# Kernel tuning notes

Measured on AMD Instinct MI355X. Metric: run time of the kernel, lower is better.

Reference implementation:

```python
import jax, jax.numpy as jnp
import numpy as np

N_NODES = 100000
D_IN = 128
D_OUT = 128
N_EDGES = 1600000
BN_EPS = 1e-5
LEAKY_SLOPE = 0.01


def setup_inputs() -> dict:
    key = jax.random.key(0)
    ks = jax.random.split(key, 8)
    x = jax.random.normal(ks[0], (N_NODES, D_IN), dtype=jnp.float32)
    edge_index = jax.random.randint(ks[1], (2, N_EDGES), 0, N_NODES, dtype=jnp.int32)
    scale = 1.0 / np.sqrt(D_IN)
    W = jax.random.uniform(ks[2], (D_IN, D_OUT), jnp.float32, -scale, scale)
    b = jax.random.uniform(ks[3], (D_OUT,), jnp.float32, -scale, scale)
    bn_gamma = jnp.ones((D_IN,), jnp.float32)
    bn_beta = jnp.zeros((D_IN,), jnp.float32)
    bn_mean = jax.random.normal(ks[4], (D_IN,), jnp.float32) * 0.01
    bn_var = jax.random.uniform(ks[5], (D_IN,), jnp.float32, 0.5, 1.5)
    rs_W = jax.random.uniform(ks[6], (D_IN, D_OUT), jnp.float32, -scale, scale)
    rs_b = jax.random.uniform(ks[7], (D_OUT,), jnp.float32, -scale, scale)
    return {"x": x, "edge_index": edge_index, "W": W, "b": b,
            "bn_gamma": bn_gamma, "bn_beta": bn_beta,
            "bn_mean": bn_mean, "bn_var": bn_var,
            "rs_W": rs_W, "rs_b": rs_b}


def reference(x, edge_index, W, b, bn_gamma, bn_beta, bn_mean, bn_var, rs_W, rs_b):
    N = x.shape[0]
    # F.normalize: row-wise L2 normalization (eps=1e-12)
    nrm = jnp.sqrt(jnp.sum(x * x, axis=1, keepdims=True))
    x = x / jnp.maximum(nrm, 1e-12)
    # BatchNorm1d (eval mode, running stats)
    x = (x - bn_mean) * jax.lax.rsqrt(bn_var + BN_EPS) * bn_gamma + bn_beta
    # GCNConv: add self-loops, symmetric normalization
    loops = jnp.arange(N, dtype=edge_index.dtype)
    src = jnp.concatenate([edge_index[0], loops])  # [E+N] source j
    dst = jnp.concatenate([edge_index[1], loops])  # [E+N] target i
    deg = jax.ops.segment_sum(jnp.ones(dst.shape, x.dtype), dst, num_segments=N)
    dinv = jax.lax.rsqrt(deg)  # self-loops guarantee deg >= 1
    norm = dinv[src] * dinv[dst]  # [E+N]
    xw = x @ W  # [N, D_OUT]
    msgs = xw[src] * norm[:, None]  # [E+N, D_OUT] gather
    out = jax.ops.segment_sum(msgs, dst, num_segments=N) + b  # scatter-add
    # residual linear on the normalized+BN'd input
    out = out + x @ rs_W + rs_b
    # LeakyReLU (dropout is identity in eval mode)
    return jnp.where(out >= 0, out, LEAKY_SLOPE * out)
```

## Files before the change

kernel.cpp:

```cpp
#include <hip/hip_runtime.h>
#include <hip/hip_fp16.h>


#define NN 100000
#define DD 128
#define EE 1600000
#define BN_EPS 1e-5f
#define SLOPE 0.01f

#define NBKT 98
#define BWID 1024
#define CAPP 20480
#define EPB  4096

struct __align__(8) H4 { __half2 a, b; };

typedef _Float16 f16x8 __attribute__((ext_vector_type(8)));
typedef float    f32x4 __attribute__((ext_vector_type(4)));

__global__ void k_prep(const float* __restrict__ W, const float* __restrict__ rsW,
                       const float* __restrict__ b, const float* __restrict__ rb,
                       __half* __restrict__ WhT, float* __restrict__ bias2,
                       int* __restrict__ gcur) {
  int blk = blockIdx.x, t = threadIdx.x;
  if (blk == 128) {
    if (t < DD) bias2[t] = b[t] + rb[t];
    if (t < NBKT) gcur[t] = t * CAPP;
    return;
  }
  float v = (t < 128) ? W[t * 128 + blk] : rsW[(t - 128) * 128 + blk];
  WhT[blk * 256 + t] = __float2half(v);
}

__global__ void k_norm_bn(const float* __restrict__ x,
                          const float* __restrict__ gamma,
                          const float* __restrict__ beta,
                          const float* __restrict__ mean,
                          const float* __restrict__ var,
                          __half* __restrict__ Ah) {
  int row = blockIdx.x * 4 + (threadIdx.x >> 6);
  int lane = threadIdx.x & 63;
  if (row >= NN) return;
  float2 v = ((const float2*)(x + (size_t)row * DD))[lane];
  float ss = v.x * v.x + v.y * v.y;
  #pragma unroll
  for (int off = 32; off > 0; off >>= 1) ss += __shfl_xor(ss, off);
  float s = 1.0f / fmaxf(sqrtf(ss), 1e-12f);
  int c = lane * 2;
  float g0 = gamma[c]     * rsqrtf(var[c]     + BN_EPS);
  float g1 = gamma[c + 1] * rsqrtf(var[c + 1] + BN_EPS);
  float ox = (v.x * s - mean[c])     * g0 + beta[c];
  float oy = (v.y * s - mean[c + 1]) * g1 + beta[c + 1];
  ((__half2*)(Ah + (size_t)row * 256 + 128))[lane] = __floats2half2_rn(ox, oy);
}

__global__ __launch_bounds__(256) void k_binA(const int* __restrict__ src,
                                              const int* __restrict__ dst,
                                              int* __restrict__ gcur,
                                              int* __restrict__ pairs) {
  __shared__ int hist[2][NBKT];
  __shared__ int cur[2][NBKT];
  int t = threadIdx.x;
  int w2 = (t >> 6) & 1;
  if (t < NBKT) { hist[0][t] = 0; hist[1][t] = 0; }
  __syncthreads();
  int e0 = blockIdx.x * EPB;
  #pragma unroll 4
  for (int i = 0; i < EPB / 256; ++i) {
    int e = e0 + i * 256 + t;
    if (e < EE) atomicAdd(&hist[w2][dst[e] >> 10], 1);
  }
  __syncthreads();
  if (t < NBKT) {
    int h0 = hist[0][t], h1 = hist[1][t];
    int b0 = atomicAdd(&gcur[t], h0 + h1);
    cur[0][t] = b0;
    cur[1][t] = b0 + h0;
  }
  __syncthreads();
  #pragma unroll 4
  for (int i = 0; i < EPB / 256; ++i) {
    int e = e0 + i * 256 + t;
    if (e < EE) {
      int d = dst[e], s = src[e];
      int bk = d >> 10;
      int r = atomicAdd(&cur[w2][bk], 1);
      pairs[r] = ((d & 1023) << 17) | s;
    }
  }
}

__global__ __launch_bounds__(1024) void k_binB(const int* __restrict__ gcur,
                                               const int* __restrict__ pairs,
                                               int* __restrict__ csr,
                                               int2* __restrict__ startdeg,
                                               float* __restrict__ dinv) {
  __shared__ int hist[BWID];
  __shared__ int excl[BWID];
  __shared__ int wsum[16];
  int b = blockIdx.x, t = threadIdx.x;
  hist[t] = 0;
  __syncthreads();
  int pbase = b * CAPP;
  int cnt = gcur[b] - pbase;
  for (int i = t; i < cnt; i += BWID)
    atomicAdd(&hist[pairs[pbase + i] >> 17], 1);
  __syncthreads();
  int v = hist[t];
  int lane = t & 63, w = t >> 6;
  int incl = v;
  #pragma unroll
  for (int off = 1; off < 64; off <<= 1) {
    int n = __shfl_up(incl, off, 64);
    if (lane >= off) incl += n;
  }
  if (lane == 63) wsum[w] = incl;
  __syncthreads();
  if (t < 16) {
    int orig = wsum[t];
    int s = orig;
    #pragma unroll
    for (int off = 1; off < 16; off <<= 1) {
      int n = __shfl_up(s, off, 64);
      if (t >= off) s += n;
    }
    wsum[t] = s - orig;
  }
  __syncthreads();
  int myexcl = (incl - v) + wsum[w];
  excl[t] = myexcl;
  int node = b * BWID + t;
  if (node < NN) {
    dinv[node] = rsqrtf((float)(v + 1));
    startdeg[node] = make_int2(pbase + myexcl, v);
  }
  __syncthreads();
  for (int i = t; i < cnt; i += BWID) {
    int p = pairs[pbase + i];
    int pos = atomicAdd(&excl[p >> 17], 1);
    csr[pbase + pos] = p & 0x1FFFF;
  }
}

__global__ void k_aggregate(__half* __restrict__ Ah,
                            const int2* __restrict__ startdeg,
                            const int* __restrict__ csr,
                            const float* __restrict__ dinv) {
  int node = blockIdx.x * 4 + (threadIdx.x >> 6);
  int lane = threadIdx.x & 63;
  int half = lane >> 5;
  int l32  = lane & 31;
  int2 sd = startdeg[node];
  int beg = sd.x, end = sd.x + sd.y;
  float di = dinv[node];
  const H4* zr = (const H4*)Ah;
  float4 acc = make_float4(0.f, 0.f, 0.f, 0.f);
  int k = beg + half;
  for (; k + 6 < end; k += 8) {
    int j0 = csr[k], j1 = csr[k + 2], j2 = csr[k + 4], j3 = csr[k + 6];
    float d0 = dinv[j0], d1 = dinv[j1], d2 = dinv[j2], d3 = dinv[j3];
    H4 a0 = zr[(size_t)j0 * 64 + 32 + l32];
    H4 a1 = zr[(size_t)j1 * 64 + 32 + l32];
    H4 a2 = zr[(size_t)j2 * 64 + 32 + l32];
    H4 a3 = zr[(size_t)j3 * 64 + 32 + l32];
    float2 f0a = __half22float2(a0.a), f0b = __half22float2(a0.b);
    float2 f1a = __half22float2(a1.a), f1b = __half22float2(a1.b);
    float2 f2a = __half22float2(a2.a), f2b = __half22float2(a2.b);
    float2 f3a = __half22float2(a3.a), f3b = __half22float2(a3.b);
    acc.x = fmaf(d0, f0a.x, fmaf(d1, f1a.x, fmaf(d2, f2a.x, fmaf(d3, f3a.x, acc.x))));
    acc.y = fmaf(d0, f0a.y, fmaf(d1, f1a.y, fmaf(d2, f2a.y, fmaf(d3, f3a.y, acc.y))));
    acc.z = fmaf(d0, f0b.x, fmaf(d1, f1b.x, fmaf(d2, f2b.x, fmaf(d3, f3b.x, acc.z))));
    acc.w = fmaf(d0, f0b.y, fmaf(d1, f1b.y, fmaf(d2, f2b.y, fmaf(d3, f3b.y, acc.w))));
  }
  for (; k < end; k += 2) {
    int j0 = csr[k];
    float d0 = dinv[j0];
    H4 a0 = zr[(size_t)j0 * 64 + 32 + l32];
    float2 f0a = __half22float2(a0.a), f0b = __half22float2(a0.b);
    acc.x = fmaf(d0, f0a.x, acc.x);
    acc.y = fmaf(d0, f0a.y, acc.y);
    acc.z = fmaf(d0, f0b.x, acc.z);
    acc.w = fmaf(d0, f0b.y, acc.w);
  }
  acc.x += __shfl_xor(acc.x, 32, 64);
  acc.y += __shfl_xor(acc.y, 32, 64);
  acc.z += __shfl_xor(acc.z, 32, 64);
  acc.w += __shfl_xor(acc.w, 32, 64);
  if (half == 0) {
    H4 zs = zr[(size_t)node * 64 + 32 + l32];
    float2 za = __half22float2(zs.a), zb2 = __half22float2(zs.b);
    H4 o;
    o.a = __floats2half2_rn((acc.x + di * za.x) * di, (acc.y + di * za.y) * di);
    o.b = __floats2half2_rn((acc.z + di * zb2.x) * di, (acc.w + di * zb2.y) * di);
    ((H4*)Ah)[(size_t)node * 64 + l32] = o;
  }
}

__global__ __launch_bounds__(256) void k_gemm(
    const __half* __restrict__ Ah, const __half* __restrict__ WhT,
    const float* __restrict__ bias2, float* __restrict__ out) {
  const int tid = threadIdx.x;
  const int w  = tid >> 6;
  const int l  = tid & 63;
  const int lm = l & 15;
  const int lk = l >> 4;
  const int row0 = blockIdx.x * 128 + w * 32;

  int rA0 = row0 + lm;
  int rA1 = row0 + 16 + lm;
  if (rA0 >= NN) rA0 = NN - 1;
  if (rA1 >= NN) rA1 = NN - 1;

  f32x4 acc0[8], acc1[8];
  #pragma unroll
  for (int c = 0; c < 8; ++c) {
    acc0[c] = (f32x4)(0.f);
    acc1[c] = (f32x4)(0.f);
  }

  const __half* a0p = Ah + (size_t)rA0 * 256 + lk * 8;
  const __half* a1p = Ah + (size_t)rA1 * 256 + lk * 8;
  const __half* bp  = WhT + (size_t)lm * 256 + lk * 8;

  #pragma unroll
  for (int ks = 0; ks < 8; ++ks) {
    f16x8 a0 = *(const f16x8*)(a0p + ks * 32);
    f16x8 a1 = *(const f16x8*)(a1p + ks * 32);
    #pragma unroll
    for (int c = 0; c < 8; ++c) {
      f16x8 b = *(const f16x8*)(bp + (size_t)c * 16 * 256 + ks * 32);
      acc0[c] = __builtin_amdgcn_mfma_f32_16x16x32_f16(a0, b, acc0[c], 0, 0, 0);
      acc1[c] = __builtin_amdgcn_mfma_f32_16x16x32_f16(a1, b, acc1[c], 0, 0, 0);
    }
  }

  int orow0 = row0 + lk * 4;
  int orow1 = row0 + 16 + lk * 4;
  #pragma unroll
  for (int c = 0; c < 8; ++c) {
    int col = c * 16 + lm;
    float bs = bias2[col];
    #pragma unroll
    for (int r = 0; r < 4; ++r) {
      int g0 = orow0 + r;
      if (g0 < NN) {
        float v = acc0[c][r] + bs;
        out[(size_t)g0 * 128 + col] = (v >= 0.f) ? v : SLOPE * v;
      }
      int g1 = orow1 + r;
      if (g1 < NN) {
        float v = acc1[c][r] + bs;
        out[(size_t)g1 * 128 + col] = (v >= 0.f) ? v : SLOPE * v;
      }
    }
  }
}

extern "C" void kernel_launch(void* const* d_in, const int* in_sizes, int n_in,
                              void* d_out, int out_size, void* d_ws, size_t ws_size,
                              hipStream_t stream) {
  const float* x     = (const float*)d_in[0];
  const int*   ei    = (const int*)d_in[1];
  const float* W     = (const float*)d_in[2];
  const float* b     = (const float*)d_in[3];
  const float* gamma = (const float*)d_in[4];
  const float* beta  = (const float*)d_in[5];
  const float* mean  = (const float*)d_in[6];
  const float* var   = (const float*)d_in[7];
  const float* rsW   = (const float*)d_in[8];
  const float* rsb   = (const float*)d_in[9];
  float* out = (float*)d_out;
  const int* src = ei;
  const int* dst = ei + EE;

  __half* Ah       = (__half*)d_ws;
  int2*   startdeg = (int2*)(Ah + (size_t)NN * 256);
  float*  dinv     = (float*)(startdeg + NN);
  int*    gcur     = (int*)(dinv + NN);
  int*    pairs    = gcur + 128;
  int*    csr      = pairs + NBKT * CAPP;
  __half* WhT      = (__half*)(csr + NBKT * CAPP);
  float*  bias2    = (float*)(WhT + 128 * 256);

  k_prep<<<129, 256, 0, stream>>>(W, rsW, b, rsb, WhT, bias2, gcur);
  k_norm_bn<<<NN / 4, 256, 0, stream>>>(x, gamma, beta, mean, var, Ah);
  k_binA<<<(EE + EPB - 1) / EPB, 256, 0, stream>>>(src, dst, gcur, pairs);
  k_binB<<<NBKT, 1024, 0, stream>>>(gcur, pairs, csr, startdeg, dinv);
  k_aggregate<<<NN / 4, 256, 0, stream>>>(Ah, startdeg, csr, dinv);
  k_gemm<<<(NN + 127) / 128, 256, 0, stream>>>(Ah, WhT, bias2, out);
}
```

Baseline: 298.2 us.

## Prescale features by dinv into compact buffer and stage edge binning in LDS

The normalize/BN kernel now runs after degree computation and also writes a dense 128-wide fp16 copy of the features prescaled by dinv. This lets aggregation skip the per-neighbor dinv gather and multiply, and it gathers from a 256-byte row stride instead of 512. Aggregation also gives each half-wave a contiguous half of the edge range with 8-wide unrolled loads. The binning kernel reads src/dst only once, caches packed pairs and bucket ids in shared memory, and uses four per-wave histograms, at the cost of more LDS and an extra buffer write.

```diff
diff --git a/kernel.cpp b/kernel.cpp
--- a/kernel.cpp
+++ b/kernel.cpp
@@ -32,60 +32,49 @@
   WhT[blk * 256 + t] = __float2half(v);
 }
 
-__global__ void k_norm_bn(const float* __restrict__ x,
-                          const float* __restrict__ gamma,
-                          const float* __restrict__ beta,
-                          const float* __restrict__ mean,
-                          const float* __restrict__ var,
-                          __half* __restrict__ Ah) {
-  int row = blockIdx.x * 4 + (threadIdx.x >> 6);
-  int lane = threadIdx.x & 63;
-  if (row >= NN) return;
-  float2 v = ((const float2*)(x + (size_t)row * DD))[lane];
-  float ss = v.x * v.x + v.y * v.y;
-  #pragma unroll
-  for (int off = 32; off > 0; off >>= 1) ss += __shfl_xor(ss, off);
-  float s = 1.0f / fmaxf(sqrtf(ss), 1e-12f);
-  int c = lane * 2;
-  float g0 = gamma[c]     * rsqrtf(var[c]     + BN_EPS);
-  float g1 = gamma[c + 1] * rsqrtf(var[c + 1] + BN_EPS);
-  float ox = (v.x * s - mean[c])     * g0 + beta[c];
-  float oy = (v.y * s - mean[c + 1]) * g1 + beta[c + 1];
-  ((__half2*)(Ah + (size_t)row * 256 + 128))[lane] = __floats2half2_rn(ox, oy);
-}
-
 __global__ __launch_bounds__(256) void k_binA(const int* __restrict__ src,
                                               const int* __restrict__ dst,
                                               int* __restrict__ gcur,
                                               int* __restrict__ pairs) {
-  __shared__ int hist[2][NBKT];
-  __shared__ int cur[2][NBKT];
+  __shared__ int hist[4][NBKT];
+  __shared__ int cur[4][NBKT];
+  __shared__ int pbuf[EPB];
+  __shared__ unsigned char bbuf[EPB];
   int t = threadIdx.x;
-  int w2 = (t >> 6) & 1;
-  if (t < NBKT) { hist[0][t] = 0; hist[1][t] = 0; }
+  int w4 = t >> 6;
+  for (int i = t; i < 4 * NBKT; i += 256) ((int*)hist)[i] = 0;
   __syncthreads();
   int e0 = blockIdx.x * EPB;
   #pragma unroll 4
   for (int i = 0; i < EPB / 256; ++i) {
-    int e = e0 + i * 256 + t;
-    if (e < EE) atomicAdd(&hist[w2][dst[e] >> 10], 1);
-  }
-  __syncthreads();
-  if (t < NBKT) {
-    int h0 = hist[0][t], h1 = hist[1][t];
-    int b0 = atomicAdd(&gcur[t], h0 + h1);
-    cur[0][t] = b0;
-    cur[1][t] = b0 + h0;
-  }
-  __syncthreads();
-  #pragma unroll 4
-  for (int i = 0; i < EPB / 256; ++i) {
-    int e = e0 + i * 256 + t;
+    int idx = i * 256 + t;
+    int e = e0 + idx;
     if (e < EE) {
       int d = dst[e], s = src[e];
       int bk = d >> 10;
-      int r = atomicAdd(&cur[w2][bk], 1);
-      pairs[r] = ((d & 1023) << 17) | s;
+      atomicAdd(&hist[w4][bk], 1);
+      pbuf[idx] = ((d & 1023) << 17) | s;
+      bbuf[idx] = (unsigned char)bk;
+    }
+  }
+  __syncthreads();
+  if (t < NBKT) {
+    int h0 = hist[0][t], h1 = hist[1][t], h2 = hist[2][t], h3 = hist[3][t];
+    int b0 = atomicAdd(&gcur[t], h0 + h1 + h2 + h3);
+    cur[0][t] = b0;
+    cur[1][t] = b0 + h0;
+    cur[2][t] = b0 + h0 + h1;
+    cur[3][t] = b0 + h0 + h1 + h2;
+  }
+  __syncthreads();
+  #pragma unroll 4
+  for (int i = 0; i < EPB / 256; ++i) {
+    int idx = i * 256 + t;
+    int e = e0 + idx;
+    if (e < EE) {
+      int bk = bbuf[idx];
+      int r = atomicAdd(&cur[w4][bk], 1);
+      pairs[r] = pbuf[idx];
     }
   }
 }
@@ -142,7 +131,33 @@
   }
 }
 
-__global__ void k_aggregate(__half* __restrict__ Ah,
+__global__ void k_norm_bn(const float* __restrict__ x,
+                          const float* __restrict__ gamma,
+                          const float* __restrict__ beta,
+                          const float* __restrict__ mean,
+                          const float* __restrict__ var,
+                          const float* __restrict__ dinv,
+                          __half* __restrict__ Ah, __half* __restrict__ zp) {
+  int row = blockIdx.x * 4 + (threadIdx.x >> 6);
+  int lane = threadIdx.x & 63;
+  if (row >= NN) return;
+  float2 v = ((const float2*)(x + (size_t)row * DD))[lane];
+  float ss = v.x * v.x + v.y * v.y;
+  #pragma unroll
+  for (int off = 32; off > 0; off >>= 1) ss += __shfl_xor(ss, off);
+  float s = 1.0f / fmaxf(sqrtf(ss), 1e-12f);
+  float di = dinv[row];
+  int c = lane * 2;
+  float g0 = gamma[c]     * rsqrtf(var[c]     + BN_EPS);
+  float g1 = gamma[c + 1] * rsqrtf(var[c + 1] + BN_EPS);
+  float ox = (v.x * s - mean[c])     * g0 + beta[c];
+  float oy = (v.y * s - mean[c + 1]) * g1 + beta[c + 1];
+  ((__half2*)(Ah + (size_t)row * 256 + 128))[lane] = __floats2half2_rn(ox, oy);
+  ((__half2*)(zp + (size_t)row * DD))[lane] = __floats2half2_rn(di * ox, di * oy);
+}
+
+__global__ void k_aggregate(const __half* __restrict__ zp,
+                            __half* __restrict__ Ah,
                             const int2* __restrict__ startdeg,
                             const int* __restrict__ csr,
                             const float* __restrict__ dinv) {
@@ -151,47 +166,41 @@
   int half = lane >> 5;
   int l32  = lane & 31;
   int2 sd = startdeg[node];
-  int beg = sd.x, end = sd.x + sd.y;
+  int mid = sd.x + (sd.y >> 1);
+  int k   = half ? mid : sd.x;
+  int end = half ? (sd.x + sd.y) : mid;
   float di = dinv[node];
-  const H4* zr = (const H4*)Ah;
+  const H4* zr = (const H4*)zp;
   float4 acc = make_float4(0.f, 0.f, 0.f, 0.f);
-  int k = beg + half;
-  for (; k + 6 < end; k += 8) {
-    int j0 = csr[k], j1 = csr[k + 2], j2 = csr[k + 4], j3 = csr[k + 6];
-    float d0 = dinv[j0], d1 = dinv[j1], d2 = dinv[j2], d3 = dinv[j3];
-    H4 a0 = zr[(size_t)j0 * 64 + 32 + l32];
-    H4 a1 = zr[(size_t)j1 * 64 + 32 + l32];
-    H4 a2 = zr[(size_t)j2 * 64 + 32 + l32];
-    H4 a3 = zr[(size_t)j3 * 64 + 32 + l32];
-    float2 f0a = __half22float2(a0.a), f0b = __half22float2(a0.b);
-    float2 f1a = __half22float2(a1.a), f1b = __half22float2(a1.b);
-    float2 f2a = __half22float2(a2.a), f2b = __half22float2(a2.b);
-    float2 f3a = __half22float2(a3.a), f3b = __half22float2(a3.b);
-    acc.x = fmaf(d0, f0a.x, fmaf(d1, f1a.x, fmaf(d2, f2a.x, fmaf(d3, f3a.x, acc.x))));
-    acc.y = fmaf(d0, f0a.y, fmaf(d1, f1a.y, fmaf(d2, f2a.y, fmaf(d3, f3a.y, acc.y))));
-    acc.z = fmaf(d0, f0b.x, fmaf(d1, f1b.x, fmaf(d2, f2b.x, fmaf(d3, f3b.x, acc.z))));
-    acc.w = fmaf(d0, f0b.y, fmaf(d1, f1b.y, fmaf(d2, f2b.y, fmaf(d3, f3b.y, acc.w))));
-  }
-  for (; k < end; k += 2) {
+  for (; k + 8 <= end; k += 8) {
+    int j[8];
+    #pragma unroll
+    for (int u = 0; u < 8; ++u) j[u] = csr[k + u];
+    H4 a[8];
+    #pragma unroll
+    for (int u = 0; u < 8; ++u) a[u] = zr[(size_t)j[u] * 32 + l32];
+    #pragma unroll
+    for (int u = 0; u < 8; ++u) {
+      float2 fa = __half22float2(a[u].a), fb = __half22float2(a[u].b);
+      acc.x += fa.x; acc.y += fa.y; acc.z += fb.x; acc.w += fb.y;
+    }
+  }
+  for (; k < end; ++k) {
     int j0 = csr[k];
-    float d0 = dinv[j0];
-    H4 a0 = zr[(size_t)j0 * 64 + 32 + l32];
-    float2 f0a = __half22float2(a0.a), f0b = __half22float2(a0.b);
-    acc.x = fmaf(d0, f0a.x, acc.x);
-    acc.y = fmaf(d0, f0a.y, acc.y);
-    acc.z = fmaf(d0, f0b.x, acc.z);
-    acc.w = fmaf(d0, f0b.y, acc.w);
+    H4 a0 = zr[(size_t)j0 * 32 + l32];
+    float2 fa = __half22float2(a0.a), fb = __half22float2(a0.b);
+    acc.x += fa.x; acc.y += fa.y; acc.z += fb.x; acc.w += fb.y;
   }
   acc.x += __shfl_xor(acc.x, 32, 64);
   acc.y += __shfl_xor(acc.y, 32, 64);
   acc.z += __shfl_xor(acc.z, 32, 64);
   acc.w += __shfl_xor(acc.w, 32, 64);
   if (half == 0) {
-    H4 zs = zr[(size_t)node * 64 + 32 + l32];
+    H4 zs = zr[(size_t)node * 32 + l32];
     float2 za = __half22float2(zs.a), zb2 = __half22float2(zs.b);
     H4 o;
-    o.a = __floats2half2_rn((acc.x + di * za.x) * di, (acc.y + di * za.y) * di);
-    o.b = __floats2half2_rn((acc.z + di * zb2.x) * di, (acc.w + di * zb2.y) * di);
+    o.a = __floats2half2_rn((acc.x + za.x) * di, (acc.y + za.y) * di);
+    o.b = __floats2half2_rn((acc.z + zb2.x) * di, (acc.w + zb2.y) * di);
     ((H4*)Ah)[(size_t)node * 64 + l32] = o;
   }
 }
@@ -274,7 +283,8 @@
   const int* dst = ei + EE;
 
   __half* Ah       = (__half*)d_ws;
-  int2*   startdeg = (int2*)(Ah + (size_t)NN * 256);
+  __half* zp       = Ah + (size_t)NN * 256;
+  int2*   startdeg = (int2*)(zp + (size_t)NN * DD);
   float*  dinv     = (float*)(startdeg + NN);
   int*    gcur     = (int*)(dinv + NN);
   int*    pairs    = gcur + 128;
@@ -283,9 +293,9 @@
   float*  bias2    = (float*)(WhT + 128 * 256);
 
   k_prep<<<129, 256, 0, stream>>>(W, rsW, b, rsb, WhT, bias2, gcur);
-  k_norm_bn<<<NN / 4, 256, 0, stream>>>(x, gamma, beta, mean, var, Ah);
   k_binA<<<(EE + EPB - 1) / EPB, 256, 0, stream>>>(src, dst, gcur, pairs);
   k_binB<<<NBKT, 1024, 0, stream>>>(gcur, pairs, csr, startdeg, dinv);
-  k_aggregate<<<NN / 4, 256, 0, stream>>>(Ah, startdeg, csr, dinv);
+  k_norm_bn<<<NN / 4, 256, 0, stream>>>(x, gamma, beta, mean, var, dinv, Ah, zp);
+  k_aggregate<<<NN / 4, 256, 0, stream>>>(zp, Ah, startdeg, csr, dinv);
   k_gemm<<<(NN + 127) / 128, 256, 0, stream>>>(Ah, WhT, bias2, out);
 }
```

After: 309.6 us. +3.8%, slower.

## Prescale features by dinv into compact buffer and stage GEMM weights in LDS

Applied to the files above, without the earlier changes.

The normalize/BN kernel now runs after degree computation and also writes a dense 128-wide fp16 copy pre-multiplied by the source node's dinv. The aggregation gathers from this compact buffer with plain adds instead of loading dinv per neighbor, which cuts random gather traffic and per-edge loads. Separately, the GEMM now uses 512-thread blocks over 256 rows, preloads A fragments into registers, and stages the whole fp16 weight matrix into swizzled 64KB shared memory instead of reading B from global memory. The cost is an extra 25.6MB buffer write and a reordered kernel schedule.

```diff
diff --git a/kernel.cpp b/kernel.cpp
--- a/kernel.cpp
+++ b/kernel.cpp
@@ -30,28 +30,6 @@
   }
   float v = (t < 128) ? W[t * 128 + blk] : rsW[(t - 128) * 128 + blk];
   WhT[blk * 256 + t] = __float2half(v);
-}
-
-__global__ void k_norm_bn(const float* __restrict__ x,
-                          const float* __restrict__ gamma,
-                          const float* __restrict__ beta,
-                          const float* __restrict__ mean,
-                          const float* __restrict__ var,
-                          __half* __restrict__ Ah) {
-  int row = blockIdx.x * 4 + (threadIdx.x >> 6);
-  int lane = threadIdx.x & 63;
-  if (row >= NN) return;
-  float2 v = ((const float2*)(x + (size_t)row * DD))[lane];
-  float ss = v.x * v.x + v.y * v.y;
-  #pragma unroll
-  for (int off = 32; off > 0; off >>= 1) ss += __shfl_xor(ss, off);
-  float s = 1.0f / fmaxf(sqrtf(ss), 1e-12f);
-  int c = lane * 2;
-  float g0 = gamma[c]     * rsqrtf(var[c]     + BN_EPS);
-  float g1 = gamma[c + 1] * rsqrtf(var[c + 1] + BN_EPS);
-  float ox = (v.x * s - mean[c])     * g0 + beta[c];
-  float oy = (v.y * s - mean[c + 1]) * g1 + beta[c + 1];
-  ((__half2*)(Ah + (size_t)row * 256 + 128))[lane] = __floats2half2_rn(ox, oy);
 }
 
 __global__ __launch_bounds__(256) void k_binA(const int* __restrict__ src,
@@ -142,7 +120,33 @@
   }
 }
 
-__global__ void k_aggregate(__half* __restrict__ Ah,
+__global__ void k_norm_bn(const float* __restrict__ x,
+                          const float* __restrict__ gamma,
+                          const float* __restrict__ beta,
+                          const float* __restrict__ mean,
+                          const float* __restrict__ var,
+                          const float* __restrict__ dinv,
+                          __half* __restrict__ Ah, __half* __restrict__ zp) {
+  int row = blockIdx.x * 4 + (threadIdx.x >> 6);
+  int lane = threadIdx.x & 63;
+  if (row >= NN) return;
+  float2 v = ((const float2*)(x + (size_t)row * DD))[lane];
+  float ss = v.x * v.x + v.y * v.y;
+  #pragma unroll
+  for (int off = 32; off > 0; off >>= 1) ss += __shfl_xor(ss, off);
+  float s = 1.0f / fmaxf(sqrtf(ss), 1e-12f);
+  float di = dinv[row];
+  int c = lane * 2;
+  float g0 = gamma[c]     * rsqrtf(var[c]     + BN_EPS);
+  float g1 = gamma[c + 1] * rsqrtf(var[c + 1] + BN_EPS);
+  float ox = (v.x * s - mean[c])     * g0 + beta[c];
+  float oy = (v.y * s - mean[c + 1]) * g1 + beta[c + 1];
+  ((__half2*)(Ah + (size_t)row * 256 + 128))[lane] = __floats2half2_rn(ox, oy);
+  ((__half2*)(zp + (size_t)row * DD))[lane] = __floats2half2_rn(di * ox, di * oy);
+}
+
+__global__ void k_aggregate(const __half* __restrict__ zp,
+                            __half* __restrict__ Ah,
                             const int2* __restrict__ startdeg,
                             const int* __restrict__ csr,
                             const float* __restrict__ dinv) {
@@ -153,64 +157,78 @@
   int2 sd = startdeg[node];
   int beg = sd.x, end = sd.x + sd.y;
   float di = dinv[node];
-  const H4* zr = (const H4*)Ah;
+  const H4* zr = (const H4*)zp;
   float4 acc = make_float4(0.f, 0.f, 0.f, 0.f);
   int k = beg + half;
   for (; k + 6 < end; k += 8) {
     int j0 = csr[k], j1 = csr[k + 2], j2 = csr[k + 4], j3 = csr[k + 6];
-    float d0 = dinv[j0], d1 = dinv[j1], d2 = dinv[j2], d3 = dinv[j3];
-    H4 a0 = zr[(size_t)j0 * 64 + 32 + l32];
-    H4 a1 = zr[(size_t)j1 * 64 + 32 + l32];
-    H4 a2 = zr[(size_t)j2 * 64 + 32 + l32];
-    H4 a3 = zr[(size_t)j3 * 64 + 32 + l32];
+    H4 a0 = zr[(size_t)j0 * 32 + l32];
+    H4 a1 = zr[(size_t)j1 * 32 + l32];
+    H4 a2 = zr[(size_t)j2 * 32 + l32];
+    H4 a3 = zr[(size_t)j3 * 32 + l32];
     float2 f0a = __half22float2(a0.a), f0b = __half22float2(a0.b);
     float2 f1a = __half22float2(a1.a), f1b = __half22float2(a1.b);
     float2 f2a = __half22float2(a2.a), f2b = __half22float2(a2.b);
     float2 f3a = __half22float2(a3.a), f3b = __half22float2(a3.b);
-    acc.x = fmaf(d0, f0a.x, fmaf(d1, f1a.x, fmaf(d2, f2a.x, fmaf(d3, f3a.x, acc.x))));
-    acc.y = fmaf(d0, f0a.y, fmaf(d1, f1a.y, fmaf(d2, f2a.y, fmaf(d3, f3a.y, acc.y))));
-    acc.z = fmaf(d0, f0b.x, fmaf(d1, f1b.x, fmaf(d2, f2b.x, fmaf(d3, f3b.x, acc.z))));
-    acc.w = fmaf(d0, f0b.y, fmaf(d1, f1b.y, fmaf(d2, f2b.y, fmaf(d3, f3b.y, acc.w))));
+    acc.x += (f0a.x + f1a.x) + (f2a.x + f3a.x);
+    acc.y += (f0a.y + f1a.y) + (f2a.y + f3a.y);
+    acc.z += (f0b.x + f1b.x) + (f2b.x + f3b.x);
+    acc.w += (f0b.y + f1b.y) + (f2b.y + f3b.y);
   }
   for (; k < end; k += 2) {
     int j0 = csr[k];
-    float d0 = dinv[j0];
-    H4 a0 = zr[(size_t)j0 * 64 + 32 + l32];
-    float2 f0a = __half22float2(a0.a), f0b = __half22float2(a0.b);
-    acc.x = fmaf(d0, f0a.x, acc.x);
-    acc.y = fmaf(d0, f0a.y, acc.y);
-    acc.z = fmaf(d0, f0b.x, acc.z);
-    acc.w = fmaf(d0, f0b.y, acc.w);
+    H4 a0 = zr[(size_t)j0 * 32 + l32];
+    float2 fa = __half22float2(a0.a), fb = __half22float2(a0.b);
+    acc.x += fa.x; acc.y += fa.y; acc.z += fb.x; acc.w += fb.y;
   }
   acc.x += __shfl_xor(acc.x, 32, 64);
   acc.y += __shfl_xor(acc.y, 32, 64);
   acc.z += __shfl_xor(acc.z, 32, 64);
   acc.w += __shfl_xor(acc.w, 32, 64);
   if (half == 0) {
-    H4 zs = zr[(size_t)node * 64 + 32 + l32];
+    H4 zs = zr[(size_t)node * 32 + l32];
     float2 za = __half22float2(zs.a), zb2 = __half22float2(zs.b);
     H4 o;
-    o.a = __floats2half2_rn((acc.x + di * za.x) * di, (acc.y + di * za.y) * di);
-    o.b = __floats2half2_rn((acc.z + di * zb2.x) * di, (acc.w + di * zb2.y) * di);
+    o.a = __floats2half2_rn((acc.x + za.x) * di, (acc.y + za.y) * di);
+    o.b = __floats2half2_rn((acc.z + zb2.x) * di, (acc.w + zb2.y) * di);
     ((H4*)Ah)[(size_t)node * 64 + l32] = o;
   }
 }
 
-__global__ __launch_bounds__(256) void k_gemm(
+__global__ __launch_bounds__(512, 2) void k_gemm(
     const __half* __restrict__ Ah, const __half* __restrict__ WhT,
     const float* __restrict__ bias2, float* __restrict__ out) {
+  __shared__ __align__(16) char Bs[65536];
   const int tid = threadIdx.x;
   const int w  = tid >> 6;
   const int l  = tid & 63;
   const int lm = l & 15;
   const int lk = l >> 4;
-  const int row0 = blockIdx.x * 128 + w * 32;
+  const int row0 = blockIdx.x * 256 + w * 32;
 
   int rA0 = row0 + lm;
   int rA1 = row0 + 16 + lm;
   if (rA0 >= NN) rA0 = NN - 1;
   if (rA1 >= NN) rA1 = NN - 1;
 
+  const __half* a0p = Ah + (size_t)rA0 * 256 + lk * 8;
+  const __half* a1p = Ah + (size_t)rA1 * 256 + lk * 8;
+  f16x8 a0[8], a1[8];
+  #pragma unroll
+  for (int ks = 0; ks < 8; ++ks) {
+    a0[ks] = *(const f16x8*)(a0p + ks * 32);
+    a1[ks] = *(const f16x8*)(a1p + ks * 32);
+  }
+
+  #pragma unroll
+  for (int i = 0; i < 8; ++i) {
+    int idx = tid + i * 512;
+    int byte = idx * 16;
+    int swz = byte ^ (((byte >> 9) & 7) << 4);
+    *(float4*)(Bs + swz) = ((const float4*)WhT)[idx];
+  }
+  __syncthreads();
+
   f32x4 acc0[8], acc1[8];
   #pragma unroll
   for (int c = 0; c < 8; ++c) {
@@ -218,19 +236,14 @@
     acc1[c] = (f32x4)(0.f);
   }
 
-  const __half* a0p = Ah + (size_t)rA0 * 256 + lk * 8;
-  const __half* a1p = Ah + (size_t)rA1 * 256 + lk * 8;
-  const __half* bp  = WhT + (size_t)lm * 256 + lk * 8;
-
   #pragma unroll
   for (int ks = 0; ks < 8; ++ks) {
-    f16x8 a0 = *(const f16x8*)(a0p + ks * 32);
-    f16x8 a1 = *(const f16x8*)(a1p + ks * 32);
     #pragma unroll
     for (int c = 0; c < 8; ++c) {
-      f16x8 b = *(const f16x8*)(bp + (size_t)c * 16 * 256 + ks * 32);
-      acc0[c] = __builtin_amdgcn_mfma_f32_16x16x32_f16(a0, b, acc0[c], 0, 0, 0);
-      acc1[c] = __builtin_amdgcn_mfma_f32_16x16x32_f16(a1, b, acc1[c], 0, 0, 0);
+      int byte = (c * 16 + lm) * 512 + lk * 16 + ks * 64;
+      f16x8 b = *(const f16x8*)(Bs + (byte ^ ((lm & 7) << 4)));
+      acc0[c] = __builtin_amdgcn_mfma_f32_16x16x32_f16(a0[ks], b, acc0[c], 0, 0, 0);
+      acc1[c] = __builtin_amdgcn_mfma_f32_16x16x32_f16(a1[ks], b, acc1[c], 0, 0, 0);
     }
   }
 
@@ -274,7 +287,8 @@
   const int* dst = ei + EE;
 
   __half* Ah       = (__half*)d_ws;
-  int2*   startdeg = (int2*)(Ah + (size_t)NN * 256);
+  __half* zp       = Ah + (size_t)NN * 256;
+  int2*   startdeg = (int2*)(zp + (size_t)NN * DD);
   float*  dinv     = (float*)(startdeg + NN);
   int*    gcur     = (int*)(dinv + NN);
   int*    pairs    = gcur + 128;
@@ -283,9 +297,9 @@
   float*  bias2    = (float*)(WhT + 128 * 256);
 
   k_prep<<<129, 256, 0, stream>>>(W, rsW, b, rsb, WhT, bias2, gcur);
-  k_norm_bn<<<NN / 4, 256, 0, stream>>>(x, gamma, beta, mean, var, Ah);
   k_binA<<<(EE + EPB - 1) / EPB, 256, 0, stream>>>(src, dst, gcur, pairs);
   k_binB<<<NBKT, 1024, 0, stream>>>(gcur, pairs, csr, startdeg, dinv);
-  k_aggregate<<<NN / 4, 256, 0, stream>>>(Ah, startdeg, csr, dinv);
-  k_gemm<<<(NN + 127) / 128, 256, 0, stream>>>(Ah, WhT, bias2, out);
-}
+  k_norm_bn<<<NN / 4, 256, 0, stream>>>(x, gamma, beta, mean, var, dinv, Ah, zp);
+  k_aggregate<<<NN / 4, 256, 0, stream>>>(zp, Ah, startdeg, csr, dinv);
+  k_gemm<<<(NN + 255) / 256, 512, 0, stream>>>(Ah, WhT, bias2, out);
+}
```

After: 281.0 us. -5.8%, faster.
